# Kernel optimization log

Hardware: AMD Instinct MI355X
Metric: run time of the kernel (lower is better)

## Reference

```python
import jax, jax.numpy as jnp
import numpy as np

D_MODEL = 1024
HEADS = 16
D_K = D_MODEL // HEADS
D_FF = 4096
B, S = 2, 2048
EPS = 1e-5


def setup_inputs() -> dict:
    key = jax.random.key(0)
    ks = jax.random.split(key, 16)
    sc_att = 1.0 / np.sqrt(D_MODEL)
    sc_ff1 = 1.0 / np.sqrt(D_MODEL)
    sc_ff2 = 1.0 / np.sqrt(D_FF)
    return {
        "input": jax.random.normal(ks[0], (B, S, D_MODEL), jnp.float32),
        "mask": jnp.ones((B, 1, 1, S), jnp.int32),
        # stacked per-head projections: [H, D_MODEL, D_K]
        "Wq": jax.random.normal(ks[1], (HEADS, D_MODEL, D_K), jnp.float32) * sc_att,
        "bq": jax.random.normal(ks[2], (HEADS, D_K), jnp.float32) * 0.01,
        "Wk": jax.random.normal(ks[3], (HEADS, D_MODEL, D_K), jnp.float32) * sc_att,
        "bk": jax.random.normal(ks[4], (HEADS, D_K), jnp.float32) * 0.01,
        "Wv": jax.random.normal(ks[5], (HEADS, D_MODEL, D_K), jnp.float32) * sc_att,
        "bv": jax.random.normal(ks[6], (HEADS, D_K), jnp.float32) * 0.01,
        "Wo": jax.random.normal(ks[7], (D_MODEL, D_MODEL), jnp.float32) * sc_att,
        "bo": jax.random.normal(ks[8], (D_MODEL,), jnp.float32) * 0.01,
        "ln1_g": jnp.ones((D_MODEL,), jnp.float32),
        "ln1_b": jnp.zeros((D_MODEL,), jnp.float32),
        "ln2_g": jnp.ones((D_MODEL,), jnp.float32),
        "ln2_b": jnp.zeros((D_MODEL,), jnp.float32),
        "W1": jax.random.normal(ks[9], (D_MODEL, D_FF), jnp.float32) * sc_ff1,
        "b1": jax.random.normal(ks[10], (D_FF,), jnp.float32) * 0.01,
        "W2": jax.random.normal(ks[11], (D_FF, D_MODEL), jnp.float32) * sc_ff2,
        "b2": jax.random.normal(ks[12], (D_MODEL,), jnp.float32) * 0.01,
    }


def _layernorm(x, g, b):
    mu = jnp.mean(x, axis=-1, keepdims=True)
    var = jnp.mean(jnp.square(x - mu), axis=-1, keepdims=True)
    return (x - mu) * jax.lax.rsqrt(var + EPS) * g + b


def reference(input, mask, Wq, bq, Wk, bk, Wv, bv, Wo, bo,
              ln1_g, ln1_b, ln2_g, ln2_b, W1, b1, W2, b2):
    x = input
    # per-head projections, stacked: [B,H,S,D_K]
    q = jnp.einsum('bsd,hdk->bhsk', x, Wq) + bq[None, :, None, :]
    k = jnp.einsum('bsd,hdk->bhsk', x, Wk) + bk[None, :, None, :]
    v = jnp.einsum('bsd,hdk->bhsk', x, Wv) + bv[None, :, None, :]
    scores = jnp.einsum('bhqk,bhsk->bhqs', q, k) / np.sqrt(D_K)  # [B,H,S,S]
    scores = jnp.where(mask == 0, jnp.float32(-1e9), scores)
    attn = jax.nn.softmax(scores, axis=-1)
    ctx = jnp.einsum('bhqs,bhsk->bhqk', attn, v)  # [B,H,S,D_K]
    # concat heads along feature dim (head h occupies slice h*D_K:(h+1)*D_K)
    ctx = jnp.transpose(ctx, (0, 2, 1, 3)).reshape(B, S, D_MODEL)
    att_out = ctx @ Wo + bo
    h = _layernorm(x + att_out, ln1_g, ln1_b)
    ff = jax.nn.relu(h @ W1 + b1) @ W2 + b2
    return _layernorm(h + ff, ln2_g, ln2_b)
```

## Files before the change

### kernel.cpp

```cpp
#include <hip/hip_runtime.h>
#include <cstdint>
#include <cstddef>

typedef unsigned short u16;
typedef unsigned int   u32;
typedef unsigned short u16x4 __attribute__((ext_vector_type(4)));
typedef unsigned short u16x8 __attribute__((ext_vector_type(8)));
typedef unsigned int   u32x2 __attribute__((ext_vector_type(2)));
typedef __bf16 bf16x8 __attribute__((ext_vector_type(8)));
typedef float f32x4 __attribute__((ext_vector_type(4)));

#define MFMA16(a, b, c) __builtin_amdgcn_mfma_f32_16x16x32_bf16((a), (b), (c), 0, 0, 0)

__device__ __forceinline__ float bf2f(u16 h) {
  union { unsigned u; float f; } v; v.u = ((unsigned)h) << 16; return v.f;
}
__device__ __forceinline__ u16 f2bf(float f) {
  union { float f; unsigned u; } v; v.f = f;
  unsigned r = v.u + 0x7fffu + ((v.u >> 16) & 1u);
  return (u16)(r >> 16);
}
__device__ __forceinline__ void gll16(const u16* g, u16* l) {
  __builtin_amdgcn_global_load_lds(
      (const __attribute__((address_space(1))) void*)g,
      (__attribute__((address_space(3))) void*)l, 16, 0, 0);
}
__device__ __forceinline__ float fast_exp2(float x) {
#if __has_builtin(__builtin_amdgcn_exp2f)
  return __builtin_amdgcn_exp2f(x);
#else
  return exp2f(x);
#endif
}

__global__ __launch_bounds__(256) void prep_all(
    const float* __restrict__ bq, const float* __restrict__ bk,
    const float* __restrict__ bv, const int* __restrict__ mask,
    float* __restrict__ biasq, float* __restrict__ madd2,
    const float* __restrict__ x, u16* __restrict__ xb,
    const float* __restrict__ Wq, const float* __restrict__ Wk,
    const float* __restrict__ Wv, u16* __restrict__ Wqkv_t,
    const float* __restrict__ Wo, const float* __restrict__ W1,
    const float* __restrict__ W2, u16* __restrict__ Wo_t,
    u16* __restrict__ W1_t, u16* __restrict__ W2_t) {
  __shared__ u16 tile[32][33];
  const int id = blockIdx.x;
  const int tid = threadIdx.x;

  if (id < 28) {
    int i = id * 256 + tid;
    if (i < 3072) {
      biasq[i] = (i < 1024) ? bq[i] * 0.18033688f
                            : (i < 2048 ? bk[i - 1024] : bv[i - 2048]);
    } else if (i < 7168) {
      int j = i - 3072;
      madd2[j] = mask[j] ? -23.083120f : -1.442695e9f;
    }
    return;
  }
  if (id < 4124) {
    int i = ((id - 28) * 256 + tid) * 4;
    const float4 v = *(const float4*)&x[i];
    u16x4 o;
    o[0] = f2bf(v.x); o[1] = f2bf(v.y); o[2] = f2bf(v.z); o[3] = f2bf(v.w);
    *(u16x4*)&xb[i] = o;
    return;
  }
  if (id < 7196) {
    int t = id - 4124;
    const int bx = t & 1, by = (t >> 1) & 31, z = t >> 6;
    const int which = z >> 4, h = z & 15;
    const float* in = (which == 0 ? Wq : (which == 1 ? Wk : Wv)) + (size_t)h * 1024 * 64;
    u16* out = Wqkv_t + ((size_t)which * 1024 + h * 64) * 1024;
    const float sc = (which == 0) ? 0.18033688f : 1.0f;
    const int tx = tid & 31, ty = tid >> 5;
    const int r0 = by * 32, c0 = bx * 32;
    #pragma unroll
    for (int i = 0; i < 32; i += 8)
      tile[ty + i][tx] = f2bf(in[(size_t)(r0 + ty + i) * 64 + c0 + tx] * sc);
    __syncthreads();
    #pragma unroll
    for (int i = 0; i < 32; i += 8)
      out[(size_t)(c0 + ty + i) * 1024 + r0 + tx] = tile[tx][ty + i];
    return;
  }
  {
    int t0 = id - 7196;
    const float* in; u16* outp; int R, C, cx, ry;
    if (t0 < 1024)      { in = Wo; outp = Wo_t; R = 1024; C = 1024; cx = t0 & 31;  ry = t0 >> 5; }
    else if (t0 < 5120) { int t = t0 - 1024; in = W1; outp = W1_t; R = 1024; C = 4096; cx = t & 127; ry = t >> 7; }
    else                { int t = t0 - 5120; in = W2; outp = W2_t; R = 4096; C = 1024; cx = t & 31;  ry = t >> 5; }
    const int tx = tid & 31, ty = tid >> 5;
    const int r0 = ry * 32, c0 = cx * 32;
    #pragma unroll
    for (int i = 0; i < 32; i += 8)
      tile[ty + i][tx] = f2bf(in[(size_t)(r0 + ty + i) * C + c0 + tx]);
    __syncthreads();
    #pragma unroll
    for (int i = 0; i < 32; i += 8)
      outp[(size_t)(c0 + ty + i) * R + r0 + tx] = tile[tx][ty + i];
  }
}

__device__ __forceinline__ void xcd_tiles(int& m0, int& n0) {
  const int gX = gridDim.x, gY = gridDim.y;
  int n = blockIdx.y * gX + blockIdx.x;
  int cpx = (gX * gY) >> 3;
  int t = (n & 7) * cpx + (n >> 3);
  n0 = (t / gY) * 128;
  m0 = (t % gY) * 128;
}
__device__ __forceinline__ void xcd_tiles256(int& m0, int& n0) {
  const int gX = gridDim.x, gY = gridDim.y;
  int n = blockIdx.y * gX + blockIdx.x;
  int cpx = (gX * gY) >> 3;
  int t = (n & 7) * cpx + (n >> 3);
  n0 = (t / gY) * 256;
  m0 = (t % gY) * 256;
}

template <int MODE>
__global__ __launch_bounds__(512, 2) void gemm256(
    const u16* __restrict__ A, const u16* __restrict__ Bt,
    const float* __restrict__ bias, u16* __restrict__ C,
    int M, int N, int K) {
  extern __shared__ __align__(16) u16 lds[];
  u16* As = lds;
  u16* Bs = lds + 2 * 256 * 64;
  const int tid = threadIdx.x;
  const int lane = tid & 63, wave = tid >> 6;
  int m0, n0;
  xcd_tiles256(m0, n0);
  const int wr = (wave >> 2) * 128;
  const int wc = (wave & 3) * 64;
  const int lrow = lane & 15, quad = lane >> 4;

  const int g_r = wave * 8 + (lane >> 3);
  const int g_c = (lane & 7) * 8;
  const u16* gA = A + (size_t)(m0 + g_r) * K + g_c;
  const u16* gB = Bt + (size_t)(n0 + g_r) * K + g_c;
  const int wbase = wave * 512;

  f32x4 acc[8][4];
  #pragma unroll
  for (int i = 0; i < 8; ++i)
    #pragma unroll
    for (int j = 0; j < 4; ++j)
      acc[i][j] = (f32x4){0.f, 0.f, 0.f, 0.f};

  const int NT = K >> 6;

  #pragma unroll
  for (int h = 0; h < 2; ++h) {
    gll16(gA + (size_t)(h * 128) * K,      As + h * 8192 + wbase);
    gll16(gA + (size_t)(h * 128 + 64) * K, As + h * 8192 + 4096 + wbase);
    gll16(gB + (size_t)(h * 128) * K,      Bs + h * 8192 + wbase);
    gll16(gB + (size_t)(h * 128 + 64) * K, Bs + h * 8192 + 4096 + wbase);
  }
  __syncthreads();

  for (int t = 0; t < NT; ++t) {
    const int p = t & 1;
    const u16* Ab = As + p * 16384;
    const u16* Bb = Bs + p * 16384;
    bf16x8 bfr[4][2];
    #pragma unroll
    for (int q = 0; q < 4; ++q) {
      if (q == 0) {
        #pragma unroll
        for (int fc = 0; fc < 4; ++fc)
          #pragma unroll
          for (int kh = 0; kh < 2; ++kh)
            bfr[fc][kh] = *(const bf16x8*)&Bb[(wc + fc * 16 + lrow) * 64 + kh * 32 + quad * 8];
      }
      bf16x8 af2[2][2];
      #pragma unroll
      for (int j = 0; j < 2; ++j)
        #pragma unroll
        for (int kh = 0; kh < 2; ++kh)
          af2[j][kh] = *(const bf16x8*)&Ab[(wr + (q * 2 + j) * 16 + lrow) * 64 + kh * 32 + quad * 8];
      if (t + 1 < NT) {
        const int kc = (t + 1) * 64;
        u16* dst = ((q < 2) ? As : Bs) + (p ^ 1) * 16384 + (q & 1) * 8192 + wbase;
        const u16* src = ((q < 2) ? gA : gB) + (size_t)((q & 1) * 128) * K + kc;
        gll16(src, dst);
        gll16(src + (size_t)64 * K, dst + 4096);
      }
      __builtin_amdgcn_s_barrier();
      #pragma unroll
      for (int j = 0; j < 2; ++j)
        #pragma unroll
        for (int fc = 0; fc < 4; ++fc) {
          acc[q * 2 + j][fc] = MFMA16(af2[j][0], bfr[fc][0], acc[q * 2 + j][fc]);
          acc[q * 2 + j][fc] = MFMA16(af2[j][1], bfr[fc][1], acc[q * 2 + j][fc]);
        }
      if (q < 3) __builtin_amdgcn_s_barrier();
    }
    __syncthreads();
  }

  #pragma unroll
  for (int fr = 0; fr < 8; ++fr) {
    int rowb = m0 + wr + fr * 16 + quad * 4;
    #pragma unroll
    for (int fc = 0; fc < 4; ++fc) {
      int col = n0 + wc + fc * 16 + lrow;
      float bv = bias[col];
      #pragma unroll
      for (int r = 0; r < 4; ++r) {
        float v = acc[fr][fc][r] + bv;
        if (MODE == 1) v = fmaxf(v, 0.f);
        C[(size_t)(rowb + r) * N + col] = f2bf(v);
      }
    }
  }
}

__global__ __launch_bounds__(256) void gemm_splitk(
    const u16* __restrict__ A, const u16* __restrict__ Bt,
    u16* __restrict__ Cp, int M, int N, int K) {
  __shared__ __align__(16) u16 As[2][128 * 32];
  __shared__ __align__(16) u16 Bs[2][128 * 32];
  const int tid = threadIdx.x;
  const int lane = tid & 63;
  const int wave = tid >> 6;
  int m0, n0;
  xcd_tiles(m0, n0);
  const int kz = blockIdx.z;
  const int Kh = K >> 1;
  const int kbase = kz * Kh;
  const int wr = (wave >> 1) * 64;
  const int wc = (wave & 1) * 64;
  const int lrow = lane & 15;
  const int quad = lane >> 4;

  const int srow = lane >> 2;
  const int scol = (lane & 3) * 8;
  const u16* gA1 = &A[(size_t)(m0 + wave * 16 + srow) * K + kbase + scol];
  const u16* gA2 = &A[(size_t)(m0 + 64 + wave * 16 + srow) * K + kbase + scol];
  const u16* gB1 = &Bt[(size_t)(n0 + wave * 16 + srow) * K + kbase + scol];
  const u16* gB2 = &Bt[(size_t)(n0 + 64 + wave * 16 + srow) * K + kbase + scol];
  const int so1 = (wave * 16) * 32;
  const int so2 = (wave * 16 + 64) * 32;
  u16* C = Cp + (size_t)kz * M * N;

  f32x4 acc[4][4];
  #pragma unroll
  for (int i = 0; i < 4; ++i)
    #pragma unroll
    for (int j = 0; j < 4; ++j)
      acc[i][j] = (f32x4){0.f, 0.f, 0.f, 0.f};

  for (int k0 = 0; k0 < Kh; k0 += 64) {
    gll16(gA1 + k0, &As[0][so1]);
    gll16(gA2 + k0, &As[0][so2]);
    gll16(gB1 + k0, &Bs[0][so1]);
    gll16(gB2 + k0, &Bs[0][so2]);
    gll16(gA1 + k0 + 32, &As[1][so1]);
    gll16(gA2 + k0 + 32, &As[1][so2]);
    gll16(gB1 + k0 + 32, &Bs[1][so1]);
    gll16(gB2 + k0 + 32, &Bs[1][so2]);
    __syncthreads();
    #pragma unroll
    for (int kb = 0; kb < 2; ++kb) {
      bf16x8 af[4], bfr[4];
      #pragma unroll
      for (int i = 0; i < 4; ++i) {
        af[i]  = *(const bf16x8*)&As[kb][(wr + i * 16 + lrow) * 32 + quad * 8];
        bfr[i] = *(const bf16x8*)&Bs[kb][(wc + i * 16 + lrow) * 32 + quad * 8];
      }
      #pragma unroll
      for (int fr = 0; fr < 4; ++fr)
        #pragma unroll
        for (int fc = 0; fc < 4; ++fc)
          acc[fr][fc] = MFMA16(af[fr], bfr[fc], acc[fr][fc]);
    }
    __syncthreads();
  }

  #pragma unroll
  for (int fr = 0; fr < 4; ++fr) {
    int rowb = m0 + wr + fr * 16 + quad * 4;
    #pragma unroll
    for (int fc = 0; fc < 4; ++fc) {
      int col = n0 + wc + fc * 16 + lrow;
      #pragma unroll
      for (int r = 0; r < 4; ++r)
        C[(size_t)(rowb + r) * N + col] = f2bf(acc[fr][fc][r]);
    }
  }
}

__global__ __launch_bounds__(256) void attn_kernel(
    const u16* __restrict__ xqkv, const float* __restrict__ madd2,
    u16* __restrict__ ctx) {
  __shared__ __align__(16) u16 Ks[64][72];
  __shared__ __align__(16) u16 Vt[64][72];
  __shared__ __align__(16) u16 Ps[4][2][16][72];
  const int tid = threadIdx.x;
  const int lane = tid & 63;
  const int wave = tid >> 6;
  const int lrow = lane & 15;
  const int quad = lane >> 4;
  const int b = blockIdx.z, h = blockIdx.y;
  const int qb = blockIdx.x * 128 + wave * 16;
  const u16* Qp = xqkv + (size_t)b * 2048 * 3072 + h * 64;
  const u16* Kp = Qp + 1024;
  const u16* Vp = Qp + 2048;

  bf16x8 qa[2][2];
  #pragma unroll
  for (int t = 0; t < 2; ++t) {
    qa[t][0] = *(const bf16x8*)&Qp[(size_t)(qb + t * 64 + lrow) * 3072 + quad * 8];
    qa[t][1] = *(const bf16x8*)&Qp[(size_t)(qb + t * 64 + lrow) * 3072 + 32 + quad * 8];
  }

  f32x4 o[2][4];
  #pragma unroll
  for (int t = 0; t < 2; ++t)
    #pragma unroll
    for (int i = 0; i < 4; ++i) o[t][i] = (f32x4){0.f, 0.f, 0.f, 0.f};
  float rsum[2] = {0.f, 0.f};

  const int ks_row = tid >> 3, ks_col = (tid & 7) * 8;
  const int v_dg = tid >> 4;
  const int v_kp = tid & 15;
  const float* maddb = madd2 + b * 2048;

  u16x8 kreg[2];
  u16x4 va[2], vb[2];
  #pragma unroll
  for (int sh = 0; sh < 2; ++sh) {
    kreg[sh] = *(const u16x8*)&Kp[(size_t)(sh * 32 + ks_row) * 3072 + ks_col];
    va[sh] = *(const u16x4*)&Vp[(size_t)(sh * 32 + 2 * v_kp) * 3072 + v_dg * 4];
    vb[sh] = *(const u16x4*)&Vp[(size_t)(sh * 32 + 2 * v_kp + 1) * 3072 + v_dg * 4];
  }

  for (int s0 = 0; s0 < 2048; s0 += 64) {
    __syncthreads();
    #pragma unroll
    for (int sh = 0; sh < 2; ++sh) {
      *(u16x8*)&Ks[sh * 32 + ks_row][ks_col] = kreg[sh];
      #pragma unroll
      for (int j = 0; j < 4; ++j) {
        u32 pk = ((u32)vb[sh][j] << 16) | (u32)va[sh][j];
        *(u32*)&Vt[v_dg * 4 + j][sh * 32 + 2 * v_kp] = pk;
      }
    }
    __syncthreads();
    if (s0 + 64 < 2048) {
      #pragma unroll
      for (int sh = 0; sh < 2; ++sh) {
        int sb = s0 + 64 + sh * 32;
        kreg[sh] = *(const u16x8*)&Kp[(size_t)(sb + ks_row) * 3072 + ks_col];
        va[sh] = *(const u16x4*)&Vp[(size_t)(sb + 2 * v_kp) * 3072 + v_dg * 4];
        vb[sh] = *(const u16x4*)&Vp[(size_t)(sb + 2 * v_kp + 1) * 3072 + v_dg * 4];
      }
    }

    bf16x8 kf[4][2], vf[4][2];
    #pragma unroll
    for (int kb = 0; kb < 4; ++kb) {
      kf[kb][0] = *(const bf16x8*)&Ks[kb * 16 + lrow][quad * 8];
      kf[kb][1] = *(const bf16x8*)&Ks[kb * 16 + lrow][32 + quad * 8];
    }
    #pragma unroll
    for (int nb = 0; nb < 4; ++nb) {
      vf[nb][0] = *(const bf16x8*)&Vt[nb * 16 + lrow][quad * 8];
      vf[nb][1] = *(const bf16x8*)&Vt[nb * 16 + lrow][32 + quad * 8];
    }

    #pragma unroll
    for (int t = 0; t < 2; ++t) {
      #pragma unroll
      for (int kb = 0; kb < 4; ++kb) {
        f32x4 z = (f32x4){0.f, 0.f, 0.f, 0.f};
        z = MFMA16(kf[kb][0], qa[t][0], z);
        z = MFMA16(kf[kb][1], qa[t][1], z);
        f32x4 m4 = *(const f32x4*)&maddb[s0 + kb * 16 + quad * 4];
        u32 pb[4];
        #pragma unroll
        for (int r = 0; r < 4; ++r) {
          float p = fast_exp2(z[r] + m4[r]);
          rsum[t] += p;
          union { float f; u32 u; } cv; cv.f = p;
          pb[r] = cv.u + 0x8000u;
        }
        u32x2 w2;
        w2[0] = __builtin_amdgcn_perm(pb[1], pb[0], 0x07060302);
        w2[1] = __builtin_amdgcn_perm(pb[3], pb[2], 0x07060302);
        *(u32x2*)&Ps[wave][t][lrow][kb * 16 + quad * 4] = w2;
      }
      #pragma unroll
      for (int kh = 0; kh < 2; ++kh) {
        bf16x8 pa = *(const bf16x8*)&Ps[wave][t][lrow][kh * 32 + quad * 8];
        #pragma unroll
        for (int nb = 0; nb < 4; ++nb)
          o[t][nb] = MFMA16(pa, vf[nb][kh], o[t][nb]);
      }
    }
  }

  #pragma unroll
  for (int t = 0; t < 2; ++t) {
    float rs = rsum[t];
    rs += __shfl_xor(rs, 16, 64);
    rs += __shfl_xor(rs, 32, 64);
    float inv = 1.f / fmaxf(rs, 1e-30f);
    #pragma unroll
    for (int r = 0; r < 4; ++r) {
      float invq = __shfl(inv, quad * 4 + r, 64);
      int q = qb + t * 64 + quad * 4 + r;
      #pragma unroll
      for (int nb = 0; nb < 4; ++nb) {
        float v = o[t][nb][r] * invq;
        ctx[((size_t)b * 2048 + q) * 1024 + h * 64 + nb * 16 + lrow] = f2bf(v);
      }
    }
  }
}

template <int IN_BF, int OUT_BF>
__global__ __launch_bounds__(256) void add_ln2p(
    const void* __restrict__ xa_, const u16* __restrict__ p0,
    const u16* __restrict__ p1, const float* __restrict__ cb,
    const float* __restrict__ g, const float* __restrict__ bb,
    void* __restrict__ outp_) {
  __shared__ float red[8];
  const int tid = threadIdx.x;
  const size_t base = (size_t)blockIdx.x * 1024;
  const float* xf = (const float*)xa_;
  const u16*   xb = (const u16*)xa_;
  float v[4];
  float s = 0.f;
  #pragma unroll
  for (int i = 0; i < 4; ++i) {
    int c = i * 256 + tid;
    float xv = IN_BF ? bf2f(xb[base + c]) : xf[base + c];
    v[i] = xv + bf2f(p0[base + c]) + bf2f(p1[base + c]) + cb[c];
    s += v[i];
  }
  #pragma unroll
  for (int off = 32; off > 0; off >>= 1) s += __shfl_down(s, off, 64);
  if ((tid & 63) == 0) red[tid >> 6] = s;
  __syncthreads();
  float mean = (red[0] + red[1] + red[2] + red[3]) * (1.f / 1024.f);
  float s2 = 0.f;
  #pragma unroll
  for (int i = 0; i < 4; ++i) { float d = v[i] - mean; s2 += d * d; }
  #pragma unroll
  for (int off = 32; off > 0; off >>= 1) s2 += __shfl_down(s2, off, 64);
  if ((tid & 63) == 0) red[4 + (tid >> 6)] = s2;
  __syncthreads();
  float var = (red[4] + red[5] + red[6] + red[7]) * (1.f / 1024.f);
  float rstd = rsqrtf(var + 1e-5f);
  #pragma unroll
  for (int i = 0; i < 4; ++i) {
    int c = i * 256 + tid;
    float r = (v[i] - mean) * rstd * g[c] + bb[c];
    if (OUT_BF) ((u16*)outp_)[base + c] = f2bf(r);
    else        ((float*)outp_)[base + c] = r;
  }
}

extern "C" void kernel_launch(void* const* d_in, const int* in_sizes, int n_in,
                              void* d_out, int out_size, void* d_ws, size_t ws_size,
                              hipStream_t stream) {
  (void)in_sizes; (void)n_in; (void)out_size; (void)ws_size;
  const float* x    = (const float*)d_in[0];
  const int*   mask = (const int*)d_in[1];
  const float* Wq   = (const float*)d_in[2];
  const float* bq   = (const float*)d_in[3];
  const float* Wk   = (const float*)d_in[4];
  const float* bk   = (const float*)d_in[5];
  const float* Wv   = (const float*)d_in[6];
  const float* bv   = (const float*)d_in[7];
  const float* Wo   = (const float*)d_in[8];
  const float* bo   = (const float*)d_in[9];
  const float* ln1g = (const float*)d_in[10];
  const float* ln1b = (const float*)d_in[11];
  const float* ln2g = (const float*)d_in[12];
  const float* ln2b = (const float*)d_in[13];
  const float* W1   = (const float*)d_in[14];
  const float* b1   = (const float*)d_in[15];
  const float* W2   = (const float*)d_in[16];
  const float* b2   = (const float*)d_in[17];
  float* out = (float*)d_out;

  char* ws = (char*)d_ws;
  u16*   Wqkv_t = (u16*)(ws + 0);
  u16*   fp     = (u16*)(ws + 0);
  u16*   Wo_t   = (u16*)(ws + 6291456);
  u16*   W1_t   = (u16*)(ws + 8388608);
  u16*   W2_t   = (u16*)(ws + 16777216);
  u16*   xqkv   = (u16*)(ws + 25165824);
  u16*   wp     = (u16*)(ws + 25165824);
  u16*   xb     = (u16*)(ws + 50331648);
  u16*   ctx    = (u16*)(ws + 50331648);
  u16*   ff1    = (u16*)(ws + 25165824);
  u16*   hbuf   = (u16*)(ws + 67108864);
  float* biasq  = (float*)(ws + 75497472);
  float* madd2  = (float*)(ws + 75509760);

  prep_all<<<16412, 256, 0, stream>>>(bq, bk, bv, mask, biasq, madd2,
                                      x, xb, Wq, Wk, Wv, Wqkv_t,
                                      Wo, W1, W2, Wo_t, W1_t, W2_t);

  gemm256<0><<<dim3(12, 16), 512, 131072, stream>>>(xb, Wqkv_t, biasq, xqkv,
                                                    4096, 3072, 1024);
  attn_kernel<<<dim3(16, 16, 2), 256, 0, stream>>>(xqkv, madd2, ctx);
  gemm_splitk<<<dim3(8, 32, 2), 256, 0, stream>>>(ctx, Wo_t, wp, 4096, 1024, 1024);
  add_ln2p<0, 1><<<4096, 256, 0, stream>>>(x, wp, wp + 4194304, bo,
                                           ln1g, ln1b, hbuf);
  gemm256<1><<<dim3(16, 16), 512, 131072, stream>>>(hbuf, W1_t, b1, ff1,
                                                    4096, 4096, 1024);
  gemm_splitk<<<dim3(8, 32, 2), 256, 0, stream>>>(ff1, W2_t, fp, 4096, 1024, 4096);
  add_ln2p<1, 0><<<4096, 256, 0, stream>>>(hbuf, fp, fp + 4194304, b2,
                                           ln2g, ln2b, out);
}
```

Baseline: 366.4 us.

## Restructure 256x256 GEMM mainloop with swizzled LDS and fine-grained vmcnt pipelining

Rewrites the gemm256 mainloop. Each wave now owns a 256x32 output strip instead of a 128x64 block. LDS staging uses an XOR swizzle on the k-chunk index to avoid bank conflicts. The single per-iteration __syncthreads is replaced by four phases, each doing a partial s_waitcnt vmcnt, a barrier, LDS reads, issuing the next tile's global-to-LDS loads, and MFMAs at raised priority (s_setprio). The aim is to overlap global loads with compute and cut LDS conflicts, at the cost of more LDS reads of A per wave and fragile hand-tuned vmcnt counts.

```diff
diff --git a/kernel.cpp b/kernel.cpp
--- a/kernel.cpp
+++ b/kernel.cpp
@@ -126,85 +126,106 @@
     int M, int N, int K) {
   extern __shared__ __align__(16) u16 lds[];
   u16* As = lds;
-  u16* Bs = lds + 2 * 256 * 64;
+  u16* Bs = lds + 32768;
   const int tid = threadIdx.x;
   const int lane = tid & 63, wave = tid >> 6;
+  const int lrow = lane & 15, quad = lane >> 4;
   int m0, n0;
   xcd_tiles256(m0, n0);
-  const int wr = (wave >> 2) * 128;
-  const int wc = (wave & 3) * 64;
-  const int lrow = lane & 15, quad = lane >> 4;
-
-  const int g_r = wave * 8 + (lane >> 3);
-  const int g_c = (lane & 7) * 8;
-  const u16* gA = A + (size_t)(m0 + g_r) * K + g_c;
-  const u16* gB = Bt + (size_t)(n0 + g_r) * K + g_c;
-  const int wbase = wave * 512;
-
-  f32x4 acc[8][4];
-  #pragma unroll
-  for (int i = 0; i < 8; ++i)
-    #pragma unroll
-    for (int j = 0; j < 4; ++j)
-      acc[i][j] = (f32x4){0.f, 0.f, 0.f, 0.f};
+
+  const int sw = lrow & 7;
+  const int srow = tid >> 3;
+  const int scol = ((tid & 7) ^ (srow & 7)) * 8;
+  const u16* gA = A  + (size_t)(m0 + srow) * K + scol;
+  const u16* gB = Bt + (size_t)(n0 + srow) * K + scol;
+  const int tid8 = tid * 8;
+
+  f32x4 acc[16][2];
+  #pragma unroll
+  for (int i = 0; i < 16; ++i) {
+    acc[i][0] = (f32x4){0.f, 0.f, 0.f, 0.f};
+    acc[i][1] = (f32x4){0.f, 0.f, 0.f, 0.f};
+  }
 
   const int NT = K >> 6;
 
   #pragma unroll
-  for (int h = 0; h < 2; ++h) {
-    gll16(gA + (size_t)(h * 128) * K,      As + h * 8192 + wbase);
-    gll16(gA + (size_t)(h * 128 + 64) * K, As + h * 8192 + 4096 + wbase);
-    gll16(gB + (size_t)(h * 128) * K,      Bs + h * 8192 + wbase);
-    gll16(gB + (size_t)(h * 128 + 64) * K, Bs + h * 8192 + 4096 + wbase);
-  }
-  __syncthreads();
-
-  for (int t = 0; t < NT; ++t) {
+  for (int s = 0; s < 4; ++s)
+    gll16(gB + (size_t)(s * 64) * K, Bs + s * 4096 + tid8);
+  #pragma unroll
+  for (int s = 0; s < 4; ++s)
+    gll16(gA + (size_t)(s * 64) * K, As + s * 4096 + tid8);
+
+#define DSA(fr, kh) (*(const bf16x8*)&Ab[((fr) * 16 + lrow) * 64 + ((((kh) * 4 + quad) ^ sw) * 8)])
+#define DSB(fc, kh) (*(const bf16x8*)&Bb[(wave * 32 + (fc) * 16 + lrow) * 64 + ((((kh) * 4 + quad) ^ sw) * 8)])
+#define STG_B(s) gll16(gB + koff + (size_t)((s) * 64) * K, Bd + (s) * 4096)
+#define STG_A(s) gll16(gA + koff + (size_t)((s) * 64) * K, Ad + (s) * 4096)
+#define KPHASE(P, VMSTR, STEXPR)                                              \
+    asm volatile("s_waitcnt " VMSTR ::: "memory");                            \
+    __builtin_amdgcn_s_barrier();                                             \
+    asm volatile("" ::: "memory");                                            \
+    {                                                                         \
+      bf16x8 af[4][2];                                                        \
+      if ((P) == 0) {                                                         \
+        _Pragma("unroll")                                                     \
+        for (int fc = 0; fc < 2; ++fc) {                                      \
+          bfr[fc][0] = DSB(fc, 0);                                            \
+          bfr[fc][1] = DSB(fc, 1);                                            \
+        }                                                                     \
+      }                                                                       \
+      _Pragma("unroll")                                                       \
+      for (int j = 0; j < 4; ++j) {                                           \
+        af[j][0] = DSA((P) * 4 + j, 0);                                       \
+        af[j][1] = DSA((P) * 4 + j, 1);                                       \
+      }                                                                       \
+      STEXPR                                                                  \
+      __builtin_amdgcn_s_setprio(1);                                          \
+      _Pragma("unroll")                                                       \
+      for (int j = 0; j < 4; ++j) {                                           \
+        _Pragma("unroll")                                                     \
+        for (int fc = 0; fc < 2; ++fc) {                                      \
+          acc[(P) * 4 + j][fc] = MFMA16(af[j][0], bfr[fc][0], acc[(P) * 4 + j][fc]); \
+          acc[(P) * 4 + j][fc] = MFMA16(af[j][1], bfr[fc][1], acc[(P) * 4 + j][fc]); \
+        }                                                                     \
+      }                                                                       \
+      __builtin_amdgcn_s_setprio(0);                                          \
+    }
+
+  for (int t = 0; t < NT - 1; ++t) {
     const int p = t & 1;
     const u16* Ab = As + p * 16384;
     const u16* Bb = Bs + p * 16384;
-    bf16x8 bfr[4][2];
-    #pragma unroll
-    for (int q = 0; q < 4; ++q) {
-      if (q == 0) {
-        #pragma unroll
-        for (int fc = 0; fc < 4; ++fc)
-          #pragma unroll
-          for (int kh = 0; kh < 2; ++kh)
-            bfr[fc][kh] = *(const bf16x8*)&Bb[(wc + fc * 16 + lrow) * 64 + kh * 32 + quad * 8];
-      }
-      bf16x8 af2[2][2];
-      #pragma unroll
-      for (int j = 0; j < 2; ++j)
-        #pragma unroll
-        for (int kh = 0; kh < 2; ++kh)
-          af2[j][kh] = *(const bf16x8*)&Ab[(wr + (q * 2 + j) * 16 + lrow) * 64 + kh * 32 + quad * 8];
-      if (t + 1 < NT) {
-        const int kc = (t + 1) * 64;
-        u16* dst = ((q < 2) ? As : Bs) + (p ^ 1) * 16384 + (q & 1) * 8192 + wbase;
-        const u16* src = ((q < 2) ? gA : gB) + (size_t)((q & 1) * 128) * K + kc;
-        gll16(src, dst);
-        gll16(src + (size_t)64 * K, dst + 4096);
-      }
-      __builtin_amdgcn_s_barrier();
-      #pragma unroll
-      for (int j = 0; j < 2; ++j)
-        #pragma unroll
-        for (int fc = 0; fc < 4; ++fc) {
-          acc[q * 2 + j][fc] = MFMA16(af2[j][0], bfr[fc][0], acc[q * 2 + j][fc]);
-          acc[q * 2 + j][fc] = MFMA16(af2[j][1], bfr[fc][1], acc[q * 2 + j][fc]);
-        }
-      if (q < 3) __builtin_amdgcn_s_barrier();
-    }
-    __syncthreads();
-  }
-
-  #pragma unroll
-  for (int fr = 0; fr < 8; ++fr) {
-    int rowb = m0 + wr + fr * 16 + quad * 4;
-    #pragma unroll
-    for (int fc = 0; fc < 4; ++fc) {
-      int col = n0 + wc + fc * 16 + lrow;
+    u16* Ad = As + (p ^ 1) * 16384 + tid8;
+    u16* Bd = Bs + (p ^ 1) * 16384 + tid8;
+    const size_t koff = (size_t)(t + 1) * 64;
+    bf16x8 bfr[2][2];
+    KPHASE(0, "vmcnt(3)", STG_B(0); STG_B(1);)
+    KPHASE(1, "vmcnt(4)", STG_B(2); STG_B(3);)
+    KPHASE(2, "vmcnt(5)", STG_A(0); STG_A(1);)
+    KPHASE(3, "vmcnt(6)", STG_A(2); STG_A(3);)
+  }
+  {
+    const int p = (NT - 1) & 1;
+    const u16* Ab = As + p * 16384;
+    const u16* Bb = Bs + p * 16384;
+    bf16x8 bfr[2][2];
+    KPHASE(0, "vmcnt(3)", )
+    KPHASE(1, "vmcnt(2)", )
+    KPHASE(2, "vmcnt(1)", )
+    KPHASE(3, "vmcnt(0)", )
+  }
+#undef DSA
+#undef DSB
+#undef STG_B
+#undef STG_A
+#undef KPHASE
+
+  #pragma unroll
+  for (int fr = 0; fr < 16; ++fr) {
+    int rowb = m0 + fr * 16 + quad * 4;
+    #pragma unroll
+    for (int fc = 0; fc < 2; ++fc) {
+      int col = n0 + wave * 32 + fc * 16 + lrow;
       float bv = bias[col];
       #pragma unroll
       for (int r = 0; r < 4; ++r) {
```

Result: faster. 347.1 us (-5.3%).
